# Kernel tuning notes

Hardware: AMD Instinct MI355X
Metric: run time of the kernel (lower is better)

## Reference

```python
import jax, jax.numpy as jnp
import numpy as np

# Perfect-tree regularization of the recursive UpDownVec graph:
#   T tactics per internal node, S siblings per tactic, L levels, branching B = T*S.
T, S, L = 2, 4, 7
B = T * S
DIM = 128
EPS = 1.0  # epsilon in AggChildrenVec
SIZES = [B ** l for l in range(L)]          # nodes per level: 1, 8, ..., 262144
OFFS = np.concatenate([[0], np.cumsum(SIZES)])
N_TOTAL = int(OFFS[-1])                      # 299593


def setup_inputs() -> dict:
    key = jax.random.key(0)
    ks = jax.random.split(key, 12)
    sc = 1.0 / np.sqrt(DIM)
    return {
        "initial_vecs": jax.random.normal(ks[0], (N_TOTAL, DIM), jnp.float32),
        "Ws": jax.random.normal(ks[1], (DIM, DIM), jnp.float32) * sc,
        "bs": jax.random.normal(ks[2], (DIM,), jnp.float32) * sc,
        "Wc": jax.random.normal(ks[3], (DIM, DIM), jnp.float32) * sc,
        "bc": jax.random.normal(ks[4], (DIM,), jnp.float32) * sc,
        "Wx": jax.random.normal(ks[5], (DIM, DIM), jnp.float32) * sc,
        "bx": jax.random.normal(ks[6], (DIM,), jnp.float32) * sc,
        "Wf": jax.random.normal(ks[7], (DIM, 2 * DIM), jnp.float32) * sc,
        "bf": jax.random.normal(ks[8], (DIM,), jnp.float32) * sc,
        "Wh": jax.random.normal(ks[9], (1, DIM), jnp.float32) * sc,
        "bh": jax.random.normal(ks[10], (1,), jnp.float32) * sc,
    }


def reference(initial_vecs, Ws, bs, Wc, bc, Wx, bx, Wf, bf, Wh, bh):
    dim = initial_vecs.shape[-1]
    init = [initial_vecs[OFFS[l]:OFFS[l + 1]] for l in range(L)]  # static slices

    # ---- up_step (bottom-up): leaves -> root ----
    agg = [None] * L
    agg[L - 1] = init[L - 1]                                    # leaves: agg = initial
    for l in range(L - 2, -1, -1):
        ch = agg[l + 1].reshape(SIZES[l], T, S, dim)            # children agg vecs
        # AggSiblingsVec: mean over siblings of relu(linear)
        sib_h = jax.nn.relu(jnp.einsum('ntsd,ed->ntse', ch, Ws) + bs)
        sib_agg = sib_h.mean(axis=2)                            # [n, T, dim]
        # AggChildrenVec: node + eps * mean over tactics of relu(linear)
        ch_h = jax.nn.relu(jnp.einsum('ntd,ed->nte', sib_agg, Wc) + bc)
        agg[l] = init[l] + EPS * ch_h.mean(axis=1)

    # ---- down_step (top-down): root -> leaves ----
    ctx = [None] * L
    ctx[0] = jnp.ones((1, dim), initial_vecs.dtype)             # root context = ones
    for l in range(L - 1):
        # AggContextVec over cat([parent_ctx, other_siblings_agg]); mean is
        # order-invariant so set-based sibling gathering is reproduced exactly.
        h = jax.nn.relu(agg[l + 1] @ Wx.T + bx).reshape(SIZES[l], T, S, dim)
        sum_h = h.sum(axis=2)                                   # [n, T, dim]
        ctx_h = jax.nn.relu(ctx[l] @ Wx.T + bx)                 # [n, dim]
        child_ctx = (ctx_h[:, None, None, :] + sum_h[:, :, None, :] - h) / S
        ctx[l + 1] = child_ctx.reshape(SIZES[l + 1], dim)

    # ---- final_agg for every node ----
    ctx_all = jnp.concatenate(ctx, axis=0)                      # [N, dim]
    agg_all = jnp.concatenate(agg, axis=0)                      # [N, dim]
    x = jnp.concatenate([ctx_all, agg_all], axis=1)             # [N, 2*dim]
    x = jax.nn.relu(x @ Wf.T + bf)
    return x @ Wh.T + bh                                        # [N, 1]
```

## Files before the change

kernel.cpp:

```cpp
#include <hip/hip_runtime.h>
#include <stdint.h>

#define DIM 128
#define LPAD 136

static constexpr long long NTOT = 299593LL;

using bf16x8 = __attribute__((ext_vector_type(8))) __bf16;
using f32x4  = __attribute__((ext_vector_type(4))) float;

__device__ __forceinline__ unsigned short f2bf(float x){
    union { float f; unsigned u; } v; v.f = x;
    unsigned r = (v.u + 0x7fffu + ((v.u >> 16) & 1u)) >> 16;
    return (unsigned short)r;
}
__device__ __forceinline__ float relu(float x){ return x > 0.f ? x : 0.f; }

__device__ __forceinline__ void load_w_lds(const unsigned short* __restrict__ wsrc,
                                           unsigned short* lds, int src_stride){
    int t = threadIdx.x;
    #pragma unroll
    for (int i = 0; i < 8; ++i){
        int idx = t + i*256;
        int row = idx >> 4, col8 = (idx & 15) << 3;
        *(uint4*)(&lds[row*LPAD + col8]) = *(const uint4*)(wsrc + row*src_stride + col8);
    }
}

__global__ __launch_bounds__(256) void prep_kernel(
    const float* __restrict__ Ws, const float* __restrict__ Wc,
    const float* __restrict__ Wx, const float* __restrict__ Wf,
    unsigned short* __restrict__ wts, unsigned short* __restrict__ ctx)
{
    int idx = blockIdx.x*256 + threadIdx.x;
    if      (idx < 16384) wts[idx] = f2bf(Ws[idx]);
    else if (idx < 32768) wts[idx] = f2bf(Wc[idx - 16384]);
    else if (idx < 49152) wts[idx] = f2bf(Wx[idx - 32768]);
    else if (idx < 81920) wts[idx] = f2bf(Wf[idx - 49152]);
    else if (idx < 82048) ctx[idx - 81920] = f2bf(1.0f);
}

__global__ __launch_bounds__(256) void leaves_kernel(
    const float* __restrict__ init, unsigned short* __restrict__ agg)
{
    long long i = (long long)blockIdx.x*256 + threadIdx.x;
    const float4 v = reinterpret_cast<const float4*>(init + 37449LL*DIM)[i];
    ushort4 o;
    o.x = f2bf(v.x); o.y = f2bf(v.y); o.z = f2bf(v.z); o.w = f2bf(v.w);
    reinterpret_cast<ushort4*>(agg + 37449LL*DIM)[i] = o;
}

__global__ __launch_bounds__(256) void up_kernel(
    const unsigned short* __restrict__ wts,
    const float* __restrict__ init,
    const float* __restrict__ bs, const float* __restrict__ bc,
    unsigned short* __restrict__ agg,
    long long child_base, long long parent_base, long long n_par)
{
    __shared__ unsigned short lds_w[128*LPAD];
    __shared__ unsigned short lds_sib[16*LPAD];

    const int t = threadIdx.x;
    const int wave = t >> 6, lane = t & 63, quad = lane >> 4, l15 = lane & 15;

    load_w_lds(wts, lds_w, 128);
    __syncthreads();

    const long long n_child = n_par * 8;
    const long long rowbase = (long long)blockIdx.x*64 + wave*16;

    f32x4 acc[8];
    #pragma unroll
    for (int i = 0; i < 8; ++i) acc[i] = f32x4{0.f,0.f,0.f,0.f};

    bf16x8 afrag[4];
    #pragma unroll
    for (int ks = 0; ks < 4; ++ks){
        long long r = rowbase + l15;
        if (r >= n_child) r = n_child - 1;
        afrag[ks] = *reinterpret_cast<const bf16x8*>(agg + (child_base + r)*DIM + ks*32 + quad*8);
    }
    #pragma unroll
    for (int ks = 0; ks < 4; ++ks){
        #pragma unroll
        for (int nt = 0; nt < 8; ++nt){
            bf16x8 bfrag = *reinterpret_cast<const bf16x8*>(&lds_w[(nt*16 + l15)*LPAD + ks*32 + quad*8]);
            acc[nt] = __builtin_amdgcn_mfma_f32_16x16x32_bf16(afrag[ks], bfrag, acc[nt], 0, 0, 0);
        }
    }
    {
        const int g = wave*4 + quad;
        #pragma unroll
        for (int nt = 0; nt < 8; ++nt){
            int col = nt*16 + l15;
            float b = bs[col];
            float s = relu(acc[nt][0]+b) + relu(acc[nt][1]+b) + relu(acc[nt][2]+b) + relu(acc[nt][3]+b);
            lds_sib[g*LPAD + col] = f2bf(s * 0.25f);
        }
    }
    __syncthreads();
    load_w_lds(wts + 16384, lds_w, 128);
    __syncthreads();

    if (wave == 0){
        f32x4 acc2[8];
        #pragma unroll
        for (int i = 0; i < 8; ++i) acc2[i] = f32x4{0.f,0.f,0.f,0.f};
        bf16x8 a2[4];
        #pragma unroll
        for (int ks = 0; ks < 4; ++ks)
            a2[ks] = *reinterpret_cast<const bf16x8*>(&lds_sib[l15*LPAD + ks*32 + quad*8]);
        #pragma unroll
        for (int ks = 0; ks < 4; ++ks){
            #pragma unroll
            for (int nt = 0; nt < 8; ++nt){
                bf16x8 bfrag = *reinterpret_cast<const bf16x8*>(&lds_w[(nt*16 + l15)*LPAD + ks*32 + quad*8]);
                acc2[nt] = __builtin_amdgcn_mfma_f32_16x16x32_bf16(a2[ks], bfrag, acc2[nt], 0, 0, 0);
            }
        }
        const long long p0 = (long long)blockIdx.x*8 + quad*2;
        const long long p1 = p0 + 1;
        #pragma unroll
        for (int nt = 0; nt < 8; ++nt){
            int col = nt*16 + l15;
            float b = bc[col];
            float r0 = relu(acc2[nt][0]+b), r1 = relu(acc2[nt][1]+b);
            float r2 = relu(acc2[nt][2]+b), r3 = relu(acc2[nt][3]+b);
            if (p0 < n_par){
                long long gr = parent_base + p0;
                agg[gr*DIM + col] = f2bf(init[gr*DIM + col] + 0.5f*(r0+r1));
            }
            if (p1 < n_par){
                long long gr = parent_base + p1;
                agg[gr*DIM + col] = f2bf(init[gr*DIM + col] + 0.5f*(r2+r3));
            }
        }
    }
}

__global__ __launch_bounds__(256) void down_kernel(
    const unsigned short* __restrict__ wts,
    const float* __restrict__ bx,
    const unsigned short* __restrict__ agg,
    unsigned short* __restrict__ ctx,
    long long parent_base, long long child_base, long long n_par)
{
    __shared__ unsigned short lds_w[128*LPAD];
    __shared__ float lds_ctxh[8*132];

    const int t = threadIdx.x;
    const int wave = t >> 6, lane = t & 63, quad = lane >> 4, l15 = lane & 15;

    load_w_lds(wts + 32768, lds_w, 128);
    __syncthreads();

    const long long n_child = n_par*8;

    if (wave == 0){
        f32x4 acc[8];
        #pragma unroll
        for (int i = 0; i < 8; ++i) acc[i] = f32x4{0.f,0.f,0.f,0.f};
        bf16x8 a[4];
        #pragma unroll
        for (int ks = 0; ks < 4; ++ks){
            long long p = (long long)blockIdx.x*8 + l15;
            if (p >= n_par) p = n_par - 1;
            a[ks] = *reinterpret_cast<const bf16x8*>(ctx + (parent_base + p)*DIM + ks*32 + quad*8);
        }
        #pragma unroll
        for (int ks = 0; ks < 4; ++ks){
            #pragma unroll
            for (int nt = 0; nt < 8; ++nt){
                bf16x8 bfrag = *reinterpret_cast<const bf16x8*>(&lds_w[(nt*16 + l15)*LPAD + ks*32 + quad*8]);
                acc[nt] = __builtin_amdgcn_mfma_f32_16x16x32_bf16(a[ks], bfrag, acc[nt], 0, 0, 0);
            }
        }
        #pragma unroll
        for (int nt = 0; nt < 8; ++nt){
            int col = nt*16 + l15;
            float b = bx[col];
            #pragma unroll
            for (int rg = 0; rg < 4; ++rg){
                int j = quad*4 + rg;
                if (j < 8) lds_ctxh[j*132 + col] = relu(acc[nt][rg] + b);
            }
        }
    }
    __syncthreads();

    f32x4 acc[8];
    #pragma unroll
    for (int i = 0; i < 8; ++i) acc[i] = f32x4{0.f,0.f,0.f,0.f};
    bf16x8 a[4];
    const long long rowbase = (long long)blockIdx.x*64 + wave*16;
    #pragma unroll
    for (int ks = 0; ks < 4; ++ks){
        long long r = rowbase + l15;
        if (r >= n_child) r = n_child - 1;
        a[ks] = *reinterpret_cast<const bf16x8*>(agg + (child_base + r)*DIM + ks*32 + quad*8);
    }
    #pragma unroll
    for (int ks = 0; ks < 4; ++ks){
        #pragma unroll
        for (int nt = 0; nt < 8; ++nt){
            bf16x8 bfrag = *reinterpret_cast<const bf16x8*>(&lds_w[(nt*16 + l15)*LPAD + ks*32 + quad*8]);
            acc[nt] = __builtin_amdgcn_mfma_f32_16x16x32_bf16(a[ks], bfrag, acc[nt], 0, 0, 0);
        }
    }
    const int p_loc = wave*2 + (quad >> 1);
    #pragma unroll
    for (int nt = 0; nt < 8; ++nt){
        int col = nt*16 + l15;
        float b = bx[col];
        float h0 = relu(acc[nt][0]+b), h1 = relu(acc[nt][1]+b);
        float h2 = relu(acc[nt][2]+b), h3 = relu(acc[nt][3]+b);
        float s = h0 + h1 + h2 + h3;
        float ch = lds_ctxh[p_loc*132 + col];
        long long r = rowbase + quad*4;
        if (r   < n_child) ctx[(child_base + r  )*DIM + col] = f2bf((ch + s - h0)*0.25f);
        if (r+1 < n_child) ctx[(child_base + r+1)*DIM + col] = f2bf((ch + s - h1)*0.25f);
        if (r+2 < n_child) ctx[(child_base + r+2)*DIM + col] = f2bf((ch + s - h2)*0.25f);
        if (r+3 < n_child) ctx[(child_base + r+3)*DIM + col] = f2bf((ch + s - h3)*0.25f);
    }
}

__global__ __launch_bounds__(256) void final_kernel(
    const unsigned short* __restrict__ wts,
    const unsigned short* __restrict__ ctx,
    const unsigned short* __restrict__ agg,
    const float* __restrict__ bf_,
    const float* __restrict__ Wh, const float* __restrict__ bh,
    float* __restrict__ out)
{
    __shared__ unsigned short lds_w[128*LPAD];
    const int t = threadIdx.x;
    const int wave = t >> 6, lane = t & 63, quad = lane >> 4, l15 = lane & 15;

    f32x4 acc[8];
    #pragma unroll
    for (int i = 0; i < 8; ++i) acc[i] = f32x4{0.f,0.f,0.f,0.f};

    const long long rowbase = (long long)blockIdx.x*64 + wave*16;

    #pragma unroll
    for (int half = 0; half < 2; ++half){
        load_w_lds(wts + 49152 + half*128, lds_w, 256);
        __syncthreads();
        const unsigned short* src = half ? agg : ctx;
        bf16x8 a[4];
        #pragma unroll
        for (int ks = 0; ks < 4; ++ks){
            long long r = rowbase + l15;
            if (r >= NTOT) r = NTOT - 1;
            a[ks] = *reinterpret_cast<const bf16x8*>(src + r*DIM + ks*32 + quad*8);
        }
        #pragma unroll
        for (int ks = 0; ks < 4; ++ks){
            #pragma unroll
            for (int nt = 0; nt < 8; ++nt){
                bf16x8 bfrag = *reinterpret_cast<const bf16x8*>(&lds_w[(nt*16 + l15)*LPAD + ks*32 + quad*8]);
                acc[nt] = __builtin_amdgcn_mfma_f32_16x16x32_bf16(a[ks], bfrag, acc[nt], 0, 0, 0);
            }
        }
        __syncthreads();
    }

    float p0 = 0.f, p1 = 0.f, p2 = 0.f, p3 = 0.f;
    #pragma unroll
    for (int nt = 0; nt < 8; ++nt){
        int col = nt*16 + l15;
        float b = bf_[col], w = Wh[col];
        p0 += relu(acc[nt][0]+b)*w;
        p1 += relu(acc[nt][1]+b)*w;
        p2 += relu(acc[nt][2]+b)*w;
        p3 += relu(acc[nt][3]+b)*w;
    }
    #pragma unroll
    for (int m = 1; m < 16; m <<= 1){
        p0 += __shfl_xor(p0, m);
        p1 += __shfl_xor(p1, m);
        p2 += __shfl_xor(p2, m);
        p3 += __shfl_xor(p3, m);
    }
    if (l15 == 0){
        float bb = bh[0];
        long long r = rowbase + quad*4;
        if (r   < NTOT) out[r  ] = p0 + bb;
        if (r+1 < NTOT) out[r+1] = p1 + bb;
        if (r+2 < NTOT) out[r+2] = p2 + bb;
        if (r+3 < NTOT) out[r+3] = p3 + bb;
    }
}

extern "C" void kernel_launch(void* const* d_in, const int* in_sizes, int n_in,
                              void* d_out, int out_size, void* d_ws, size_t ws_size,
                              hipStream_t stream)
{
    const float* init = (const float*)d_in[0];
    const float* Ws  = (const float*)d_in[1];
    const float* bs  = (const float*)d_in[2];
    const float* Wc  = (const float*)d_in[3];
    const float* bc  = (const float*)d_in[4];
    const float* Wx  = (const float*)d_in[5];
    const float* bx  = (const float*)d_in[6];
    const float* Wf  = (const float*)d_in[7];
    const float* bff = (const float*)d_in[8];
    const float* Wh  = (const float*)d_in[9];
    const float* bh  = (const float*)d_in[10];
    float* out = (float*)d_out;

    unsigned short* agg = (unsigned short*)d_ws;
    unsigned short* ctx = agg + NTOT*DIM;
    unsigned short* wts = ctx + NTOT*DIM;

    static const long long SZ[7] = {1,8,64,512,4096,32768,262144};
    static const long long OF[8] = {0,1,9,73,585,4681,37449,299593};

    prep_kernel<<<dim3(321), dim3(256), 0, stream>>>(Ws, Wc, Wx, Wf, wts, ctx);
    leaves_kernel<<<dim3(32768), dim3(256), 0, stream>>>(init, agg);

    for (int l = 5; l >= 0; --l){
        int blocks = (int)((SZ[l]*8 + 63)/64);
        up_kernel<<<dim3(blocks), dim3(256), 0, stream>>>(
            wts, init, bs, bc, agg, OF[l+1], OF[l], SZ[l]);
    }
    for (int l = 0; l < 6; ++l){
        int blocks = (int)((SZ[l]*8 + 63)/64);
        down_kernel<<<dim3(blocks), dim3(256), 0, stream>>>(
            wts, bx, agg, ctx, OF[l], OF[l+1], SZ[l]);
    }
    final_kernel<<<dim3((int)((NTOT + 63)/64)), dim3(256), 0, stream>>>(
        wts, ctx, agg, bff, Wh, bh, out);
}
```

Measured before the change: 444.4 us.

## Process two row tiles per wave and fuse leaf bf16 conversion into up pass

Each wave now handles 32 rows instead of 16, so every LDS weight fragment feeds two MFMAs and the per-block weight loads are amortized over twice as many rows. The separate leaves_kernel is removed: the first up pass reads fp32 leaf inputs, converts them to bf16 in registers, and writes them to agg while using them directly. It also switches to native __bf16 conversion and adds a launch_bounds occupancy hint. In exchange it raises register pressure and halves the number of blocks, which may cut parallelism on the small levels.

```diff
diff --git a/kernel.cpp b/kernel.cpp
--- a/kernel.cpp
+++ b/kernel.cpp
@@ -9,15 +9,15 @@
 using bf16x8 = __attribute__((ext_vector_type(8))) __bf16;
 using f32x4  = __attribute__((ext_vector_type(4))) float;
 
-__device__ __forceinline__ unsigned short f2bf(float x){
-    union { float f; unsigned u; } v; v.f = x;
-    unsigned r = (v.u + 0x7fffu + ((v.u >> 16) & 1u)) >> 16;
-    return (unsigned short)r;
-}
 __device__ __forceinline__ float relu(float x){ return x > 0.f ? x : 0.f; }
-
-__device__ __forceinline__ void load_w_lds(const unsigned short* __restrict__ wsrc,
-                                           unsigned short* lds, int src_stride){
+__device__ __forceinline__ __bf16 tobf(float x){ return (__bf16)x; }
+
+__device__ __forceinline__ void mfma_acc(f32x4& acc, bf16x8 a, bf16x8 b){
+    acc = __builtin_amdgcn_mfma_f32_16x16x32_bf16(a, b, acc, 0, 0, 0);
+}
+
+__device__ __forceinline__ void load_w_lds(const __bf16* __restrict__ wsrc,
+                                           __bf16* lds, int src_stride){
     int t = threadIdx.x;
     #pragma unroll
     for (int i = 0; i < 8; ++i){
@@ -30,149 +30,159 @@
 __global__ __launch_bounds__(256) void prep_kernel(
     const float* __restrict__ Ws, const float* __restrict__ Wc,
     const float* __restrict__ Wx, const float* __restrict__ Wf,
-    unsigned short* __restrict__ wts, unsigned short* __restrict__ ctx)
+    __bf16* __restrict__ wts, __bf16* __restrict__ ctx)
 {
     int idx = blockIdx.x*256 + threadIdx.x;
-    if      (idx < 16384) wts[idx] = f2bf(Ws[idx]);
-    else if (idx < 32768) wts[idx] = f2bf(Wc[idx - 16384]);
-    else if (idx < 49152) wts[idx] = f2bf(Wx[idx - 32768]);
-    else if (idx < 81920) wts[idx] = f2bf(Wf[idx - 49152]);
-    else if (idx < 82048) ctx[idx - 81920] = f2bf(1.0f);
-}
-
-__global__ __launch_bounds__(256) void leaves_kernel(
-    const float* __restrict__ init, unsigned short* __restrict__ agg)
-{
-    long long i = (long long)blockIdx.x*256 + threadIdx.x;
-    const float4 v = reinterpret_cast<const float4*>(init + 37449LL*DIM)[i];
-    ushort4 o;
-    o.x = f2bf(v.x); o.y = f2bf(v.y); o.z = f2bf(v.z); o.w = f2bf(v.w);
-    reinterpret_cast<ushort4*>(agg + 37449LL*DIM)[i] = o;
-}
-
-__global__ __launch_bounds__(256) void up_kernel(
-    const unsigned short* __restrict__ wts,
+    if      (idx < 16384) wts[idx] = tobf(Ws[idx]);
+    else if (idx < 32768) wts[idx] = tobf(Wc[idx - 16384]);
+    else if (idx < 49152) wts[idx] = tobf(Wx[idx - 32768]);
+    else if (idx < 81920) wts[idx] = tobf(Wf[idx - 49152]);
+    else if (idx < 82048) ctx[idx - 81920] = tobf(1.0f);
+}
+
+template<bool LEAF>
+__global__ __launch_bounds__(256, 3) void up_kernel(
+    const __bf16* __restrict__ wts,
     const float* __restrict__ init,
     const float* __restrict__ bs, const float* __restrict__ bc,
-    unsigned short* __restrict__ agg,
+    __bf16* __restrict__ agg,
     long long child_base, long long parent_base, long long n_par)
 {
-    __shared__ unsigned short lds_w[128*LPAD];
-    __shared__ unsigned short lds_sib[16*LPAD];
+    __shared__ __bf16 lds_w[128*LPAD];
+    __shared__ __bf16 lds_sib[32*LPAD];
 
     const int t = threadIdx.x;
-    const int wave = t >> 6, lane = t & 63, quad = lane >> 4, l15 = lane & 15;
+    const int w = t >> 6, lane = t & 63, quad = lane >> 4, l15 = lane & 15;
 
     load_w_lds(wts, lds_w, 128);
     __syncthreads();
 
     const long long n_child = n_par * 8;
-    const long long rowbase = (long long)blockIdx.x*64 + wave*16;
-
-    f32x4 acc[8];
-    #pragma unroll
-    for (int i = 0; i < 8; ++i) acc[i] = f32x4{0.f,0.f,0.f,0.f};
-
-    bf16x8 afrag[4];
+    const long long rowbase = (long long)blockIdx.x*128 + w*32;
+
+    f32x4 acc[2][8];
+    #pragma unroll
+    for (int tt = 0; tt < 2; ++tt)
+        #pragma unroll
+        for (int i = 0; i < 8; ++i) acc[tt][i] = f32x4{0.f,0.f,0.f,0.f};
+
+    bf16x8 af[2][4];
+    #pragma unroll
+    for (int tt = 0; tt < 2; ++tt){
+        long long r = rowbase + tt*16 + l15;
+        if (r >= n_child) r = n_child - 1;
+        const long long base = (child_base + r)*DIM;
+        #pragma unroll
+        for (int ks = 0; ks < 4; ++ks){
+            if (LEAF){
+                const float* p = init + base + ks*32 + quad*8;
+                float4 v0 = *(const float4*)p;
+                float4 v1 = *(const float4*)(p + 4);
+                bf16x8 a;
+                a[0]=tobf(v0.x); a[1]=tobf(v0.y); a[2]=tobf(v0.z); a[3]=tobf(v0.w);
+                a[4]=tobf(v1.x); a[5]=tobf(v1.y); a[6]=tobf(v1.z); a[7]=tobf(v1.w);
+                af[tt][ks] = a;
+                *(uint4*)(agg + base + ks*32 + quad*8) = *(uint4*)&a;
+            } else {
+                af[tt][ks] = *(const bf16x8*)(agg + base + ks*32 + quad*8);
+            }
+        }
+    }
     #pragma unroll
     for (int ks = 0; ks < 4; ++ks){
-        long long r = rowbase + l15;
-        if (r >= n_child) r = n_child - 1;
-        afrag[ks] = *reinterpret_cast<const bf16x8*>(agg + (child_base + r)*DIM + ks*32 + quad*8);
-    }
-    #pragma unroll
-    for (int ks = 0; ks < 4; ++ks){
-        #pragma unroll
-        for (int nt = 0; nt < 8; ++nt){
-            bf16x8 bfrag = *reinterpret_cast<const bf16x8*>(&lds_w[(nt*16 + l15)*LPAD + ks*32 + quad*8]);
-            acc[nt] = __builtin_amdgcn_mfma_f32_16x16x32_bf16(afrag[ks], bfrag, acc[nt], 0, 0, 0);
-        }
-    }
-    {
-        const int g = wave*4 + quad;
+        #pragma unroll
+        for (int nt = 0; nt < 8; ++nt){
+            bf16x8 bfrag = *(const bf16x8*)&lds_w[(nt*16 + l15)*LPAD + ks*32 + quad*8];
+            mfma_acc(acc[0][nt], af[0][ks], bfrag);
+            mfma_acc(acc[1][nt], af[1][ks], bfrag);
+        }
+    }
+    #pragma unroll
+    for (int tt = 0; tt < 2; ++tt){
+        const int g = w*8 + tt*4 + quad;
         #pragma unroll
         for (int nt = 0; nt < 8; ++nt){
             int col = nt*16 + l15;
             float b = bs[col];
-            float s = relu(acc[nt][0]+b) + relu(acc[nt][1]+b) + relu(acc[nt][2]+b) + relu(acc[nt][3]+b);
-            lds_sib[g*LPAD + col] = f2bf(s * 0.25f);
+            float s = relu(acc[tt][nt][0]+b) + relu(acc[tt][nt][1]+b)
+                    + relu(acc[tt][nt][2]+b) + relu(acc[tt][nt][3]+b);
+            lds_sib[g*LPAD + col] = tobf(s * 0.25f);
         }
     }
     __syncthreads();
     load_w_lds(wts + 16384, lds_w, 128);
     __syncthreads();
 
-    if (wave == 0){
-        f32x4 acc2[8];
-        #pragma unroll
-        for (int i = 0; i < 8; ++i) acc2[i] = f32x4{0.f,0.f,0.f,0.f};
+    if (w < 2){
+        f32x4 a2c[8];
+        #pragma unroll
+        for (int i = 0; i < 8; ++i) a2c[i] = f32x4{0.f,0.f,0.f,0.f};
         bf16x8 a2[4];
         #pragma unroll
         for (int ks = 0; ks < 4; ++ks)
-            a2[ks] = *reinterpret_cast<const bf16x8*>(&lds_sib[l15*LPAD + ks*32 + quad*8]);
+            a2[ks] = *(const bf16x8*)&lds_sib[(w*16 + l15)*LPAD + ks*32 + quad*8];
         #pragma unroll
         for (int ks = 0; ks < 4; ++ks){
             #pragma unroll
             for (int nt = 0; nt < 8; ++nt){
-                bf16x8 bfrag = *reinterpret_cast<const bf16x8*>(&lds_w[(nt*16 + l15)*LPAD + ks*32 + quad*8]);
-                acc2[nt] = __builtin_amdgcn_mfma_f32_16x16x32_bf16(a2[ks], bfrag, acc2[nt], 0, 0, 0);
-            }
-        }
-        const long long p0 = (long long)blockIdx.x*8 + quad*2;
+                bf16x8 bfrag = *(const bf16x8*)&lds_w[(nt*16 + l15)*LPAD + ks*32 + quad*8];
+                mfma_acc(a2c[nt], a2[ks], bfrag);
+            }
+        }
+        const long long p0 = (long long)blockIdx.x*16 + w*8 + quad*2;
         const long long p1 = p0 + 1;
         #pragma unroll
         for (int nt = 0; nt < 8; ++nt){
             int col = nt*16 + l15;
             float b = bc[col];
-            float r0 = relu(acc2[nt][0]+b), r1 = relu(acc2[nt][1]+b);
-            float r2 = relu(acc2[nt][2]+b), r3 = relu(acc2[nt][3]+b);
+            float r0 = relu(a2c[nt][0]+b), r1 = relu(a2c[nt][1]+b);
+            float r2 = relu(a2c[nt][2]+b), r3 = relu(a2c[nt][3]+b);
             if (p0 < n_par){
                 long long gr = parent_base + p0;
-                agg[gr*DIM + col] = f2bf(init[gr*DIM + col] + 0.5f*(r0+r1));
+                agg[gr*DIM + col] = tobf(init[gr*DIM + col] + 0.5f*(r0+r1));
             }
             if (p1 < n_par){
                 long long gr = parent_base + p1;
-                agg[gr*DIM + col] = f2bf(init[gr*DIM + col] + 0.5f*(r2+r3));
-            }
-        }
-    }
-}
-
-__global__ __launch_bounds__(256) void down_kernel(
-    const unsigned short* __restrict__ wts,
+                agg[gr*DIM + col] = tobf(init[gr*DIM + col] + 0.5f*(r2+r3));
+            }
+        }
+    }
+}
+
+__global__ __launch_bounds__(256, 3) void down_kernel(
+    const __bf16* __restrict__ wts,
     const float* __restrict__ bx,
-    const unsigned short* __restrict__ agg,
-    unsigned short* __restrict__ ctx,
+    const __bf16* __restrict__ agg,
+    __bf16* __restrict__ ctx,
     long long parent_base, long long child_base, long long n_par)
 {
-    __shared__ unsigned short lds_w[128*LPAD];
-    __shared__ float lds_ctxh[8*132];
+    __shared__ __bf16 lds_w[128*LPAD];
+    __shared__ float lds_ctxh[16*132];
 
     const int t = threadIdx.x;
-    const int wave = t >> 6, lane = t & 63, quad = lane >> 4, l15 = lane & 15;
+    const int w = t >> 6, lane = t & 63, quad = lane >> 4, l15 = lane & 15;
 
     load_w_lds(wts + 32768, lds_w, 128);
     __syncthreads();
 
     const long long n_child = n_par*8;
 
-    if (wave == 0){
+    if (w == 0){
         f32x4 acc[8];
         #pragma unroll
         for (int i = 0; i < 8; ++i) acc[i] = f32x4{0.f,0.f,0.f,0.f};
         bf16x8 a[4];
+        long long p = (long long)blockIdx.x*16 + l15;
+        if (p >= n_par) p = n_par - 1;
+        #pragma unroll
+        for (int ks = 0; ks < 4; ++ks)
+            a[ks] = *(const bf16x8*)(ctx + (parent_base + p)*DIM + ks*32 + quad*8);
         #pragma unroll
         for (int ks = 0; ks < 4; ++ks){
-            long long p = (long long)blockIdx.x*8 + l15;
-            if (p >= n_par) p = n_par - 1;
-            a[ks] = *reinterpret_cast<const bf16x8*>(ctx + (parent_base + p)*DIM + ks*32 + quad*8);
-        }
-        #pragma unroll
-        for (int ks = 0; ks < 4; ++ks){
             #pragma unroll
             for (int nt = 0; nt < 8; ++nt){
-                bf16x8 bfrag = *reinterpret_cast<const bf16x8*>(&lds_w[(nt*16 + l15)*LPAD + ks*32 + quad*8]);
-                acc[nt] = __builtin_amdgcn_mfma_f32_16x16x32_bf16(a[ks], bfrag, acc[nt], 0, 0, 0);
+                bf16x8 bfrag = *(const bf16x8*)&lds_w[(nt*16 + l15)*LPAD + ks*32 + quad*8];
+                mfma_acc(acc[nt], a[ks], bfrag);
             }
         }
         #pragma unroll
@@ -180,115 +190,129 @@
             int col = nt*16 + l15;
             float b = bx[col];
             #pragma unroll
-            for (int rg = 0; rg < 4; ++rg){
-                int j = quad*4 + rg;
-                if (j < 8) lds_ctxh[j*132 + col] = relu(acc[nt][rg] + b);
-            }
-        }
-    }
-    __syncthreads();
-
-    f32x4 acc[8];
-    #pragma unroll
-    for (int i = 0; i < 8; ++i) acc[i] = f32x4{0.f,0.f,0.f,0.f};
-    bf16x8 a[4];
-    const long long rowbase = (long long)blockIdx.x*64 + wave*16;
+            for (int rg = 0; rg < 4; ++rg)
+                lds_ctxh[(quad*4 + rg)*132 + col] = relu(acc[nt][rg] + b);
+        }
+    }
+    __syncthreads();
+
+    f32x4 acc[2][8];
+    #pragma unroll
+    for (int tt = 0; tt < 2; ++tt)
+        #pragma unroll
+        for (int i = 0; i < 8; ++i) acc[tt][i] = f32x4{0.f,0.f,0.f,0.f};
+    bf16x8 a[2][4];
+    const long long rowbase = (long long)blockIdx.x*128 + w*32;
+    #pragma unroll
+    for (int tt = 0; tt < 2; ++tt){
+        long long r = rowbase + tt*16 + l15;
+        if (r >= n_child) r = n_child - 1;
+        #pragma unroll
+        for (int ks = 0; ks < 4; ++ks)
+            a[tt][ks] = *(const bf16x8*)(agg + (child_base + r)*DIM + ks*32 + quad*8);
+    }
     #pragma unroll
     for (int ks = 0; ks < 4; ++ks){
-        long long r = rowbase + l15;
-        if (r >= n_child) r = n_child - 1;
-        a[ks] = *reinterpret_cast<const bf16x8*>(agg + (child_base + r)*DIM + ks*32 + quad*8);
-    }
-    #pragma unroll
-    for (int ks = 0; ks < 4; ++ks){
-        #pragma unroll
-        for (int nt = 0; nt < 8; ++nt){
-            bf16x8 bfrag = *reinterpret_cast<const bf16x8*>(&lds_w[(nt*16 + l15)*LPAD + ks*32 + quad*8]);
-            acc[nt] = __builtin_amdgcn_mfma_f32_16x16x32_bf16(a[ks], bfrag, acc[nt], 0, 0, 0);
-        }
-    }
-    const int p_loc = wave*2 + (quad >> 1);
-    #pragma unroll
-    for (int nt = 0; nt < 8; ++nt){
-        int col = nt*16 + l15;
-        float b = bx[col];
-        float h0 = relu(acc[nt][0]+b), h1 = relu(acc[nt][1]+b);
-        float h2 = relu(acc[nt][2]+b), h3 = relu(acc[nt][3]+b);
-        float s = h0 + h1 + h2 + h3;
-        float ch = lds_ctxh[p_loc*132 + col];
-        long long r = rowbase + quad*4;
-        if (r   < n_child) ctx[(child_base + r  )*DIM + col] = f2bf((ch + s - h0)*0.25f);
-        if (r+1 < n_child) ctx[(child_base + r+1)*DIM + col] = f2bf((ch + s - h1)*0.25f);
-        if (r+2 < n_child) ctx[(child_base + r+2)*DIM + col] = f2bf((ch + s - h2)*0.25f);
-        if (r+3 < n_child) ctx[(child_base + r+3)*DIM + col] = f2bf((ch + s - h3)*0.25f);
-    }
-}
-
-__global__ __launch_bounds__(256) void final_kernel(
-    const unsigned short* __restrict__ wts,
-    const unsigned short* __restrict__ ctx,
-    const unsigned short* __restrict__ agg,
+        #pragma unroll
+        for (int nt = 0; nt < 8; ++nt){
+            bf16x8 bfrag = *(const bf16x8*)&lds_w[(nt*16 + l15)*LPAD + ks*32 + quad*8];
+            mfma_acc(acc[0][nt], a[0][ks], bfrag);
+            mfma_acc(acc[1][nt], a[1][ks], bfrag);
+        }
+    }
+    #pragma unroll
+    for (int tt = 0; tt < 2; ++tt){
+        const long long rb = rowbase + tt*16 + quad*4;
+        const int p_loc = w*4 + tt*2 + (quad >> 1);
+        #pragma unroll
+        for (int nt = 0; nt < 8; ++nt){
+            int col = nt*16 + l15;
+            float b = bx[col];
+            float h0 = relu(acc[tt][nt][0]+b), h1 = relu(acc[tt][nt][1]+b);
+            float h2 = relu(acc[tt][nt][2]+b), h3 = relu(acc[tt][nt][3]+b);
+            float s = h0 + h1 + h2 + h3;
+            float ch = lds_ctxh[p_loc*132 + col];
+            if (rb   < n_child) ctx[(child_base + rb  )*DIM + col] = tobf((ch + s - h0)*0.25f);
+            if (rb+1 < n_child) ctx[(child_base + rb+1)*DIM + col] = tobf((ch + s - h1)*0.25f);
+            if (rb+2 < n_child) ctx[(child_base + rb+2)*DIM + col] = tobf((ch + s - h2)*0.25f);
+            if (rb+3 < n_child) ctx[(child_base + rb+3)*DIM + col] = tobf((ch + s - h3)*0.25f);
+        }
+    }
+}
+
+__global__ __launch_bounds__(256, 3) void final_kernel(
+    const __bf16* __restrict__ wts,
+    const __bf16* __restrict__ ctx,
+    const __bf16* __restrict__ agg,
     const float* __restrict__ bf_,
     const float* __restrict__ Wh, const float* __restrict__ bh,
     float* __restrict__ out)
 {
-    __shared__ unsigned short lds_w[128*LPAD];
+    __shared__ __bf16 lds_w[128*LPAD];
     const int t = threadIdx.x;
-    const int wave = t >> 6, lane = t & 63, quad = lane >> 4, l15 = lane & 15;
-
-    f32x4 acc[8];
-    #pragma unroll
-    for (int i = 0; i < 8; ++i) acc[i] = f32x4{0.f,0.f,0.f,0.f};
-
-    const long long rowbase = (long long)blockIdx.x*64 + wave*16;
+    const int w = t >> 6, lane = t & 63, quad = lane >> 4, l15 = lane & 15;
+
+    f32x4 acc[2][8];
+    #pragma unroll
+    for (int tt = 0; tt < 2; ++tt)
+        #pragma unroll
+        for (int i = 0; i < 8; ++i) acc[tt][i] = f32x4{0.f,0.f,0.f,0.f};
+
+    const long long rowbase = (long long)blockIdx.x*128 + w*32;
 
     #pragma unroll
     for (int half = 0; half < 2; ++half){
         load_w_lds(wts + 49152 + half*128, lds_w, 256);
         __syncthreads();
-        const unsigned short* src = half ? agg : ctx;
-        bf16x8 a[4];
+        const __bf16* src = half ? agg : ctx;
+        bf16x8 a[2][4];
+        #pragma unroll
+        for (int tt = 0; tt < 2; ++tt){
+            long long r = rowbase + tt*16 + l15;
+            if (r >= NTOT) r = NTOT - 1;
+            #pragma unroll
+            for (int ks = 0; ks < 4; ++ks)
+                a[tt][ks] = *(const bf16x8*)(src + r*DIM + ks*32 + quad*8);
+        }
         #pragma unroll
         for (int ks = 0; ks < 4; ++ks){
-            long long r = rowbase + l15;
-            if (r >= NTOT) r = NTOT - 1;
-            a[ks] = *reinterpret_cast<const bf16x8*>(src + r*DIM + ks*32 + quad*8);
-        }
-        #pragma unroll
-        for (int ks = 0; ks < 4; ++ks){
             #pragma unroll
             for (int nt = 0; nt < 8; ++nt){
-                bf16x8 bfrag = *reinterpret_cast<const bf16x8*>(&lds_w[(nt*16 + l15)*LPAD + ks*32 + quad*8]);
-                acc[nt] = __builtin_amdgcn_mfma_f32_16x16x32_bf16(a[ks], bfrag, acc[nt], 0, 0, 0);
+                bf16x8 bfrag = *(const bf16x8*)&lds_w[(nt*16 + l15)*LPAD + ks*32 + quad*8];
+                mfma_acc(acc[0][nt], a[0][ks], bfrag);
+                mfma_acc(acc[1][nt], a[1][ks], bfrag);
             }
         }
         __syncthreads();
     }
 
-    float p0 = 0.f, p1 = 0.f, p2 = 0.f, p3 = 0.f;
-    #pragma unroll
-    for (int nt = 0; nt < 8; ++nt){
-        int col = nt*16 + l15;
-        float b = bf_[col], w = Wh[col];
-        p0 += relu(acc[nt][0]+b)*w;
-        p1 += relu(acc[nt][1]+b)*w;
-        p2 += relu(acc[nt][2]+b)*w;
-        p3 += relu(acc[nt][3]+b)*w;
-    }
-    #pragma unroll
-    for (int m = 1; m < 16; m <<= 1){
-        p0 += __shfl_xor(p0, m);
-        p1 += __shfl_xor(p1, m);
-        p2 += __shfl_xor(p2, m);
-        p3 += __shfl_xor(p3, m);
-    }
-    if (l15 == 0){
-        float bb = bh[0];
-        long long r = rowbase + quad*4;
-        if (r   < NTOT) out[r  ] = p0 + bb;
-        if (r+1 < NTOT) out[r+1] = p1 + bb;
-        if (r+2 < NTOT) out[r+2] = p2 + bb;
-        if (r+3 < NTOT) out[r+3] = p3 + bb;
+    #pragma unroll
+    for (int tt = 0; tt < 2; ++tt){
+        float p0 = 0.f, p1 = 0.f, p2 = 0.f, p3 = 0.f;
+        #pragma unroll
+        for (int nt = 0; nt < 8; ++nt){
+            int col = nt*16 + l15;
+            float b = bf_[col], wh = Wh[col];
+            p0 += relu(acc[tt][nt][0]+b)*wh;
+            p1 += relu(acc[tt][nt][1]+b)*wh;
+            p2 += relu(acc[tt][nt][2]+b)*wh;
+            p3 += relu(acc[tt][nt][3]+b)*wh;
+        }
+        #pragma unroll
+        for (int m = 1; m < 16; m <<= 1){
+            p0 += __shfl_xor(p0, m);
+            p1 += __shfl_xor(p1, m);
+            p2 += __shfl_xor(p2, m);
+            p3 += __shfl_xor(p3, m);
+        }
+        if (l15 == 0){
+            float bb = bh[0];
+            long long r = rowbase + tt*16 + quad*4;
+            if (r   < NTOT) out[r  ] = p0 + bb;
+            if (r+1 < NTOT) out[r+1] = p1 + bb;
+            if (r+2 < NTOT) out[r+2] = p2 + bb;
+            if (r+3 < NTOT) out[r+3] = p3 + bb;
+        }
     }
 }
 
@@ -309,26 +333,29 @@
     const float* bh  = (const float*)d_in[10];
     float* out = (float*)d_out;
 
-    unsigned short* agg = (unsigned short*)d_ws;
-    unsigned short* ctx = agg + NTOT*DIM;
-    unsigned short* wts = ctx + NTOT*DIM;
+    __bf16* agg = (__bf16*)d_ws;
+    __bf16* ctx = agg + NTOT*DIM;
+    __bf16* wts = ctx + NTOT*DIM;
 
     static const long long SZ[7] = {1,8,64,512,4096,32768,262144};
     static const long long OF[8] = {0,1,9,73,585,4681,37449,299593};
 
     prep_kernel<<<dim3(321), dim3(256), 0, stream>>>(Ws, Wc, Wx, Wf, wts, ctx);
-    leaves_kernel<<<dim3(32768), dim3(256), 0, stream>>>(init, agg);
 
     for (int l = 5; l >= 0; --l){
-        int blocks = (int)((SZ[l]*8 + 63)/64);
-        up_kernel<<<dim3(blocks), dim3(256), 0, stream>>>(
-            wts, init, bs, bc, agg, OF[l+1], OF[l], SZ[l]);
+        int blocks = (int)((SZ[l]*8 + 127)/128);
+        if (l == 5)
+            up_kernel<true><<<dim3(blocks), dim3(256), 0, stream>>>(
+                wts, init, bs, bc, agg, OF[6], OF[5], SZ[5]);
+        else
+            up_kernel<false><<<dim3(blocks), dim3(256), 0, stream>>>(
+                wts, init, bs, bc, agg, OF[l+1], OF[l], SZ[l]);
     }
     for (int l = 0; l < 6; ++l){
-        int blocks = (int)((SZ[l]*8 + 63)/64);
+        int blocks = (int)((SZ[l]*8 + 127)/128);
         down_kernel<<<dim3(blocks), dim3(256), 0, stream>>>(
             wts, bx, agg, ctx, OF[l], OF[l+1], SZ[l]);
     }
-    final_kernel<<<dim3((int)((NTOT + 63)/64)), dim3(256), 0, stream>>>(
+    final_kernel<<<dim3((int)((NTOT + 127)/128)), dim3(256), 0, stream>>>(
         wts, ctx, agg, bff, Wh, bh, out);
 }
```

After: 424.5 us. -4.5%, faster.
